# Kernel tuning notes

Measured on AMD Instinct MI355X. Metric: run time of the kernel, lower is better.

The kernel has to match this reference:

```python
import jax, jax.numpy as jnp
import numpy as np

B, S, C, V, LAT, NL = 256, 512, 256, 32, 256, 7
DILS = [1, 2, 4, 8, 16, 32, 64]
EPS = 1e-5


def setup_inputs() -> dict:
    key = jax.random.key(0)
    ks = jax.random.split(key, 24)
    s = 0.05
    inp = {
        "x": jax.random.randint(ks[0], (B, S), 0, V, dtype=jnp.int64 if jax.config.read("jax_enable_x64") else jnp.int32),
        "z": jax.random.normal(ks[1], (B, LAT), dtype=jnp.float32),
        "emb": jax.random.normal(ks[2], (V, C), dtype=jnp.float32) * s,
        "latent_W": jax.random.normal(ks[3], (LAT, C), dtype=jnp.float32) * s,
        "latent_b": jnp.zeros((C,), jnp.float32),
        "ln1_g": jnp.ones((NL, C), jnp.float32),
        "ln1_b": jnp.zeros((NL, C), jnp.float32),
        "w1": jax.random.normal(ks[4], (NL, C, C), jnp.float32) * s,
        "b1": jnp.zeros((NL, C), jnp.float32),
        "ln2_g": jnp.ones((NL, C), jnp.float32),
        "ln2_b": jnp.zeros((NL, C), jnp.float32),
        "wd": jax.random.normal(ks[5], (NL, 2, C, C), jnp.float32) * s,  # tap 0 = x[t-d], tap 1 = x[t]
        "bd": jnp.zeros((NL, C), jnp.float32),
        "ln3_g": jnp.ones((NL, C), jnp.float32),
        "ln3_b": jnp.zeros((NL, C), jnp.float32),
        "we": jax.random.normal(ks[6], (NL, C, C), jnp.float32) * s,
        "be": jnp.zeros((NL, C), jnp.float32),
        "wg": jax.random.normal(ks[7], (NL, C, C), jnp.float32) * s,
        "bg": jnp.zeros((NL, C), jnp.float32),
        "out_W": jax.random.normal(ks[8], (C, V), jnp.float32) * s,
        "out_b": jnp.zeros((V,), jnp.float32),
    }
    return inp


def _ln(h, g, b):
    mu = h.mean(-1, keepdims=True)
    var = jnp.mean((h - mu) ** 2, axis=-1, keepdims=True)
    return (h - mu) * jax.lax.rsqrt(var + EPS) * g + b


def _lrelu(h):
    return jnp.where(h >= 0, h, 0.01 * h)


def reference(x, z, emb, latent_W, latent_b, ln1_g, ln1_b, w1, b1,
              ln2_g, ln2_b, wd, bd, ln3_g, ln3_b, we, be, wg, bg,
              out_W, out_b):
    # channel-last layout [B, S, C] throughout (fuses away the torch transposes)
    h = emb[x] + (z @ latent_W + latent_b)[:, None, :]
    for i, d in enumerate(DILS):
        x_inp = h
        t = _lrelu(_ln(x_inp, ln1_g[i], ln1_b[i]))
        t = t @ w1[i] + b1[i]
        t = _lrelu(_ln(t, ln2_g[i], ln2_b[i]))
        # causal dilated conv, kernel=2: out[t] = W0*x[t-d] + W1*x[t]
        t_shift = jnp.pad(t, ((0, 0), (d, 0), (0, 0)))[:, :t.shape[1], :]
        t = t_shift @ wd[i, 0] + t @ wd[i, 1] + bd[i]
        t = _lrelu(_ln(t, ln3_g[i], ln3_b[i]))
        gated = (t @ we[i] + be[i]) * jax.nn.sigmoid(t @ wg[i] + bg[i])
        h = gated + x_inp
    logits = h @ out_W + out_b                      # [B, S, V]
    lp = jax.nn.log_softmax(logits, axis=-1)
    # gather log-prob of next token: lp[:, :-1, :] at x[:, 1:]
    return jnp.take_along_axis(lp[:, :-1, :], x[:, 1:, None], axis=2)[..., 0]
```

## Files before the change

### kernel.cpp

```cpp
#include <hip/hip_runtime.h>

typedef unsigned short u16;
typedef unsigned int   u32;
typedef __attribute__((ext_vector_type(8))) short short8;
typedef __attribute__((ext_vector_type(4))) float f32x4;

struct __align__(8) u16x4 { u16 x, y, z, w; };

#define NL 7
#define M_DIM 131072

__device__ __forceinline__ float b2f(u16 u) {
  union { float f; u32 i; } c; c.i = ((u32)u) << 16; return c.f;
}
__device__ __forceinline__ u16 f2b(float f) {
  union { float f; u32 i; } c; c.f = f;
  u32 r = c.i + 0x7FFFu + ((c.i >> 16) & 1u);
  return (u16)(r >> 16);
}
__device__ __forceinline__ void gload16(const void* g, void* l) {
  __builtin_amdgcn_global_load_lds((const __attribute__((address_space(1))) void*)g,
                                   (__attribute__((address_space(3))) void*)l, 16, 0, 0);
}


__global__ __launch_bounds__(256) void conv_w1_k(const float* __restrict__ w1, u16* __restrict__ wT) {
  int idx = blockIdx.x * 256 + threadIdx.x;
  int i = idx >> 16, rem = idx & 65535;
  int n = rem >> 8, k = rem & 255;
  wT[idx] = f2b(w1[(i << 16) + (k << 8) + n]);
}

__global__ __launch_bounds__(256) void conv_wd_k(const float* __restrict__ wd, u16* __restrict__ wT) {
  int idx = blockIdx.x * 256 + threadIdx.x;
  int i = idx / 131072, rem = idx & 131071;
  int n = rem >> 9, k2 = rem & 511;
  int tap = k2 >> 8, k = k2 & 255;
  wT[idx] = f2b(wd[(((i * 2 + tap) << 8) + k) * 256 + n]);
}

__global__ __launch_bounds__(256) void conv_weg_k(const float* __restrict__ we, const float* __restrict__ wg,
                                                  u16* __restrict__ wT) {
  int idx = blockIdx.x * 256 + threadIdx.x;
  int i = idx / 131072, rem = idx & 131071;
  int src = rem >> 16, n = (rem >> 8) & 255, k = rem & 255;
  const float* W = src ? wg : we;
  wT[idx] = f2b(W[((i << 8) + k) * 256 + n]);
}

__global__ __launch_bounds__(256) void conv_wo_k(const float* __restrict__ outW, u16* __restrict__ wTo) {
  int idx = blockIdx.x * 256 + threadIdx.x;
  int v = idx >> 8, k = idx & 255;
  wTo[idx] = f2b(outW[k * 32 + v]);
}


__global__ __launch_bounds__(256) void zlat_k(const float* __restrict__ z, const float* __restrict__ W,
                                              const float* __restrict__ bias, float* __restrict__ zlat) {
  int b = blockIdx.x, c = threadIdx.x;
  float acc = bias[c];
  for (int l = 0; l < 256; ++l) acc += z[b * 256 + l] * W[l * 256 + c];
  zlat[b * 256 + c] = acc;
}


__global__ __launch_bounds__(256) void embed_k(const int* __restrict__ x, const float* __restrict__ emb,
                                               const float* __restrict__ zlat, u16* __restrict__ h) {
  int wave = threadIdx.x >> 6, lane = threadIdx.x & 63;
  int r = blockIdx.x * 4 + wave;
  int c = lane * 4;
  int tok = x[r];
  int bi = r >> 9;
  float4 ev = *(const float4*)&emb[tok * 256 + c];
  float4 zv = *(const float4*)&zlat[bi * 256 + c];
  u16x4 hb;
  hb.x = f2b(ev.x + zv.x); hb.y = f2b(ev.y + zv.y);
  hb.z = f2b(ev.z + zv.z); hb.w = f2b(ev.w + zv.w);
  *(u16x4*)&h[(long)r * 256 + c] = hb;
}


__global__ __launch_bounds__(256, 2) void gemm1_k(
    const u16* __restrict__ h, const u16* __restrict__ WT,
    const float* __restrict__ ln1g, const float* __restrict__ ln1b,
    const float* __restrict__ bias,
    const float* __restrict__ ln2g, const float* __restrict__ ln2b,
    u16* __restrict__ V)
{
  __shared__ __align__(16) u16 lA[64 * 264];
  __shared__ __align__(16) u16 lB[256 * 32];
  __shared__ float pS[64][4], pQ[64][4];
  __shared__ float muA[64], rsA[64];
  const int tid = threadIdx.x;
  const int lane = tid & 63;
  const int wv = tid >> 6;
  const int wc = wv * 64;
  const int m0 = blockIdx.x * 64;
  const int rA = tid >> 2;
  const int cSw = ((((tid & 3) - ((tid >> 3) & 3)) & 3)) * 8;
  const int lr = lane & 15;
  const int quad = lane >> 4;
  const int lq = quad * 8;
  const int sw = ((quad + ((lr >> 1) & 3)) & 3) * 8;

  {
    const int half = lane >> 5, l5 = lane & 31;
    float4 ga = *(const float4*)&ln1g[l5 * 8];
    float4 gb = *(const float4*)&ln1g[l5 * 8 + 4];
    float4 ba = *(const float4*)&ln1b[l5 * 8];
    float4 bb = *(const float4*)&ln1b[l5 * 8 + 4];
    #pragma unroll 4
    for (int it = 0; it < 8; ++it) {
      int row = wv * 16 + it * 2 + half;
      uint4 hv = *(const uint4*)(h + (long)(m0 + row) * 256 + l5 * 8);
      float v0 = b2f((u16)(hv.x & 0xffff)), v1 = b2f((u16)(hv.x >> 16));
      float v2 = b2f((u16)(hv.y & 0xffff)), v3 = b2f((u16)(hv.y >> 16));
      float v4 = b2f((u16)(hv.z & 0xffff)), v5 = b2f((u16)(hv.z >> 16));
      float v6 = b2f((u16)(hv.w & 0xffff)), v7 = b2f((u16)(hv.w >> 16));
      float s = v0 + v1 + v2 + v3 + v4 + v5 + v6 + v7;
      float q = v0*v0 + v1*v1 + v2*v2 + v3*v3 + v4*v4 + v5*v5 + v6*v6 + v7*v7;
      #pragma unroll
      for (int o = 1; o < 32; o <<= 1) { s += __shfl_xor(s, o); q += __shfl_xor(q, o); }
      float mu = s * 0.00390625f;
      float var = q * 0.00390625f - mu * mu;
      float rs = rsqrtf(var + 1e-5f);
      float y0 = (v0 - mu) * rs * ga.x + ba.x; y0 = y0 >= 0.f ? y0 : 0.01f * y0;
      float y1 = (v1 - mu) * rs * ga.y + ba.y; y1 = y1 >= 0.f ? y1 : 0.01f * y1;
      float y2 = (v2 - mu) * rs * ga.z + ba.z; y2 = y2 >= 0.f ? y2 : 0.01f * y2;
      float y3 = (v3 - mu) * rs * ga.w + ba.w; y3 = y3 >= 0.f ? y3 : 0.01f * y3;
      float y4 = (v4 - mu) * rs * gb.x + bb.x; y4 = y4 >= 0.f ? y4 : 0.01f * y4;
      float y5 = (v5 - mu) * rs * gb.y + bb.y; y5 = y5 >= 0.f ? y5 : 0.01f * y5;
      float y6 = (v6 - mu) * rs * gb.z + bb.z; y6 = y6 >= 0.f ? y6 : 0.01f * y6;
      float y7 = (v7 - mu) * rs * gb.w + bb.w; y7 = y7 >= 0.f ? y7 : 0.01f * y7;
      uint4 ov;
      ov.x = (u32)f2b(y0) | ((u32)f2b(y1) << 16);
      ov.y = (u32)f2b(y2) | ((u32)f2b(y3) << 16);
      ov.z = (u32)f2b(y4) | ((u32)f2b(y5) << 16);
      ov.w = (u32)f2b(y6) | ((u32)f2b(y7) << 16);
      *(uint4*)&lA[row * 264 + l5 * 8] = ov;
    }
  }

  f32x4 acc[4][4];
  #pragma unroll
  for (int i = 0; i < 4; ++i)
    #pragma unroll
    for (int j = 0; j < 4; ++j) {
      acc[i][j][0] = 0.f; acc[i][j][1] = 0.f; acc[i][j][2] = 0.f; acc[i][j][3] = 0.f;
    }

  for (int kt = 0; kt < 8; ++kt) {
    const int kk = kt * 32;
    const long bofs = (long)rA * 256 + kk + cSw;
    #pragma unroll
    for (int j = 0; j < 4; ++j)
      gload16(WT + bofs + (long)(64 * j) * 256, &lB[tid * 8 + j * 2048]);
    __syncthreads();

    short8 af[4], bfr[4];
    #pragma unroll
    for (int mt = 0; mt < 4; ++mt)
      af[mt] = *(const short8*)&lA[(mt * 16 + lr) * 264 + kk + lq];
    #pragma unroll
    for (int nt = 0; nt < 4; ++nt)
      bfr[nt] = *(const short8*)&lB[(wc + nt * 16 + lr) * 32 + sw];
    #pragma unroll
    for (int mt = 0; mt < 4; ++mt)
      #pragma unroll
      for (int nt = 0; nt < 4; ++nt)
        acc[mt][nt] = __builtin_amdgcn_mfma_f32_16x16x32_bf16(af[mt], bfr[nt], acc[mt][nt], 0, 0, 0);
    __syncthreads();
  }

  float biasv[4], gv[4], bv[4];
  #pragma unroll
  for (int nt = 0; nt < 4; ++nt) {
    int n = wc + nt * 16 + lr;
    biasv[nt] = bias[n]; gv[nt] = ln2g[n]; bv[nt] = ln2b[n];
  }
  #pragma unroll
  for (int mt = 0; mt < 4; ++mt)
    #pragma unroll
    for (int r = 0; r < 4; ++r) {
      float s = 0.f, q = 0.f;
      #pragma unroll
      for (int nt = 0; nt < 4; ++nt) {
        float v = acc[mt][nt][r] + biasv[nt];
        acc[mt][nt][r] = v;
        s += v; q += v * v;
      }
      #pragma unroll
      for (int o = 1; o < 16; o <<= 1) { s += __shfl_xor(s, o); q += __shfl_xor(q, o); }
      if (lr == 0) { pS[mt * 16 + quad * 4 + r][wv] = s; pQ[mt * 16 + quad * 4 + r][wv] = q; }
    }
  __syncthreads();
  if (tid < 64) {
    float S = pS[tid][0] + pS[tid][1] + pS[tid][2] + pS[tid][3];
    float Q = pQ[tid][0] + pQ[tid][1] + pQ[tid][2] + pQ[tid][3];
    float mu = S * 0.00390625f;
    float var = Q * 0.00390625f - mu * mu;
    muA[tid] = mu; rsA[tid] = rsqrtf(var + 1e-5f);
  }
  __syncthreads();
  #pragma unroll
  for (int mt = 0; mt < 4; ++mt)
    #pragma unroll
    for (int r = 0; r < 4; ++r) {
      int row = mt * 16 + quad * 4 + r;
      float mu = muA[row], rs = rsA[row];
      #pragma unroll
      for (int nt = 0; nt < 4; ++nt) {
        float y = (acc[mt][nt][r] - mu) * rs * gv[nt] + bv[nt];
        y = y >= 0.f ? y : 0.01f * y;
        V[(long)(m0 + row) * 256 + wc + nt * 16 + lr] = f2b(y);
      }
    }
}


__global__ __launch_bounds__(512, 4) void gemm_ln_k(
    const u16* __restrict__ A, const u16* __restrict__ WT, int Ktot, int dil,
    const float* __restrict__ bias, const float* __restrict__ g, const float* __restrict__ b,
    u16* __restrict__ Out)
{
  __shared__ u16 lA[128 * 32];
  __shared__ u16 lB[256 * 32];
  __shared__ float pS[128][4], pQ[128][4];
  __shared__ float muA[128], rsA[128];
  const int tid = threadIdx.x;
  const int lane = tid & 63;
  const int wv = tid >> 6;
  const int mw = wv >> 2;
  const int nw = wv & 3;
  const int m0 = blockIdx.x * 128;
  const int rA = tid >> 2;
  const int cSw = ((((tid & 3) - ((tid >> 3) & 3)) & 3)) * 8;
  const int mm = m0 + rA;
  const int s1 = mm & 511;
  const bool fixBlk = (dil > 0) && ((m0 & 511) == 0);
  const int lr = lane & 15;
  const int quad = lane >> 4;
  const int sw = ((quad + ((lr >> 1) & 3)) & 3) * 8;

  f32x4 acc[4][4];
  #pragma unroll
  for (int i = 0; i < 4; ++i)
    #pragma unroll
    for (int j = 0; j < 4; ++j) {
      acc[i][j][0] = 0.f; acc[i][j][1] = 0.f; acc[i][j][2] = 0.f; acc[i][j][3] = 0.f;
    }

  const int nkt = Ktot >> 5;
  for (int kt = 0; kt < nkt; ++kt) {
    const int kk = (kt & 7) * 32;
    int r = mm;
    if (dil > 0 && kt < 8) r = (s1 >= dil) ? (mm - dil) : mm;
    gload16(A + (long)r * 256 + kk + cSw, &lA[tid * 8]);
    const u16* bSrc = WT + kt * 32 + cSw;
    gload16(bSrc + (long)rA * Ktot,         &lB[tid * 8]);
    gload16(bSrc + (long)(rA + 128) * Ktot, &lB[tid * 8 + 4096]);
    __syncthreads();

    if (fixBlk && kt < 8) {
      if (rA < dil) {
        uint4 zz; zz.x = 0; zz.y = 0; zz.z = 0; zz.w = 0;
        *(uint4*)&lA[rA * 32 + (tid & 3) * 8] = zz;
      }
      __syncthreads();
    }

    short8 af[4], bfr[4];
    #pragma unroll
    for (int mt = 0; mt < 4; ++mt)
      af[mt] = *(const short8*)&lA[(mw * 64 + mt * 16 + lr) * 32 + sw];
    #pragma unroll
    for (int nt = 0; nt < 4; ++nt)
      bfr[nt] = *(const short8*)&lB[(nw * 64 + nt * 16 + lr) * 32 + sw];
    #pragma unroll
    for (int mt = 0; mt < 4; ++mt)
      #pragma unroll
      for (int nt = 0; nt < 4; ++nt)
        acc[mt][nt] = __builtin_amdgcn_mfma_f32_16x16x32_bf16(af[mt], bfr[nt], acc[mt][nt], 0, 0, 0);
    __syncthreads();
  }

  float biasv[4], gv[4], bv[4];
  #pragma unroll
  for (int nt = 0; nt < 4; ++nt) {
    int n = nw * 64 + nt * 16 + lr;
    biasv[nt] = bias[n]; gv[nt] = g[n]; bv[nt] = b[n];
  }
  #pragma unroll
  for (int mt = 0; mt < 4; ++mt)
    #pragma unroll
    for (int r = 0; r < 4; ++r) {
      float s = 0.f, q = 0.f;
      #pragma unroll
      for (int nt = 0; nt < 4; ++nt) {
        float v = acc[mt][nt][r] + biasv[nt];
        acc[mt][nt][r] = v;
        s += v; q += v * v;
      }
      #pragma unroll
      for (int off = 1; off < 16; off <<= 1) {
        s += __shfl_xor(s, off); q += __shfl_xor(q, off);
      }
      if (lr == 0) {
        int row = mw * 64 + mt * 16 + quad * 4 + r;
        pS[row][nw] = s; pQ[row][nw] = q;
      }
    }
  __syncthreads();
  if (tid < 128) {
    float S = pS[tid][0] + pS[tid][1] + pS[tid][2] + pS[tid][3];
    float Q = pQ[tid][0] + pQ[tid][1] + pQ[tid][2] + pQ[tid][3];
    float mu = S * 0.00390625f;
    float var = Q * 0.00390625f - mu * mu;
    muA[tid] = mu; rsA[tid] = rsqrtf(var + 1e-5f);
  }
  __syncthreads();
  #pragma unroll
  for (int mt = 0; mt < 4; ++mt)
    #pragma unroll
    for (int r = 0; r < 4; ++r) {
      int row = mw * 64 + mt * 16 + quad * 4 + r;
      float mu = muA[row], rs = rsA[row];
      #pragma unroll
      for (int nt = 0; nt < 4; ++nt) {
        float y = (acc[mt][nt][r] - mu) * rs * gv[nt] + bv[nt];
        y = y >= 0.f ? y : 0.01f * y;
        Out[(long)(m0 + row) * 256 + nw * 64 + nt * 16 + lr] = f2b(y);
      }
    }
}


__global__ __launch_bounds__(256, 2) void gate_k(
    const u16* __restrict__ P, const u16* __restrict__ WTe, const u16* __restrict__ WTg,
    const float* __restrict__ be, const float* __restrict__ bg, u16* __restrict__ h)
{
  __shared__ u16 lA[64 * 32];
  __shared__ u16 lBe[256 * 32];
  __shared__ u16 lBg[256 * 32];
  const int tid = threadIdx.x;
  const int lane = tid & 63;
  const int wv = tid >> 6;
  const int wc = wv * 64;
  const int m0 = blockIdx.x * 64;
  const int rA = tid >> 2;
  const int cSw = ((((tid & 3) - ((tid >> 3) & 3)) & 3)) * 8;
  const int lr = lane & 15;
  const int quad = lane >> 4;
  const int sw = ((quad + ((lr >> 1) & 3)) & 3) * 8;

  f32x4 accE[4][4], accG[4][4];
  #pragma unroll
  for (int i = 0; i < 4; ++i)
    #pragma unroll
    for (int j = 0; j < 4; ++j) {
      accE[i][j][0] = 0.f; accE[i][j][1] = 0.f; accE[i][j][2] = 0.f; accE[i][j][3] = 0.f;
      accG[i][j][0] = 0.f; accG[i][j][1] = 0.f; accG[i][j][2] = 0.f; accG[i][j][3] = 0.f;
    }

  for (int kt = 0; kt < 8; ++kt) {
    const int kk = kt * 32;
    gload16(P + (long)(m0 + rA) * 256 + kk + cSw, &lA[tid * 8]);
    const long bofs = (long)rA * 256 + kk + cSw;
    #pragma unroll
    for (int j = 0; j < 4; ++j) {
      gload16(WTe + bofs + (long)(64 * j) * 256, &lBe[tid * 8 + j * 2048]);
      gload16(WTg + bofs + (long)(64 * j) * 256, &lBg[tid * 8 + j * 2048]);
    }
    __syncthreads();

    short8 af[4], bfe[4], bfg[4];
    #pragma unroll
    for (int mt = 0; mt < 4; ++mt)
      af[mt] = *(const short8*)&lA[(mt * 16 + lr) * 32 + sw];
    #pragma unroll
    for (int nt = 0; nt < 4; ++nt) {
      bfe[nt] = *(const short8*)&lBe[(wc + nt * 16 + lr) * 32 + sw];
      bfg[nt] = *(const short8*)&lBg[(wc + nt * 16 + lr) * 32 + sw];
    }
    #pragma unroll
    for (int mt = 0; mt < 4; ++mt)
      #pragma unroll
      for (int nt = 0; nt < 4; ++nt) {
        accE[mt][nt] = __builtin_amdgcn_mfma_f32_16x16x32_bf16(af[mt], bfe[nt], accE[mt][nt], 0, 0, 0);
        accG[mt][nt] = __builtin_amdgcn_mfma_f32_16x16x32_bf16(af[mt], bfg[nt], accG[mt][nt], 0, 0, 0);
      }
    __syncthreads();
  }

  float bev[4], bgv[4];
  #pragma unroll
  for (int nt = 0; nt < 4; ++nt) {
    int n = wc + nt * 16 + lr;
    bev[nt] = be[n]; bgv[nt] = bg[n];
  }
  #pragma unroll
  for (int mt = 0; mt < 4; ++mt)
    #pragma unroll
    for (int r = 0; r < 4; ++r) {
      int row = mt * 16 + quad * 4 + r;
      long off = (long)(m0 + row) * 256;
      #pragma unroll
      for (int nt = 0; nt < 4; ++nt) {
        int n = wc + nt * 16 + lr;
        float e = accE[mt][nt][r] + bev[nt];
        float gg = accG[mt][nt][r] + bgv[nt];
        float hn = e * (1.f / (1.f + expf(-gg))) + b2f(h[off + n]);
        h[off + n] = f2b(hn);
      }
    }
}


__global__ __launch_bounds__(256) void final_k(const u16* __restrict__ h, const u16* __restrict__ WTo,
                                               const float* __restrict__ outb, const int* __restrict__ x,
                                               float* __restrict__ out) {
  __shared__ u16 lW[32 * 264];
  const int tid = threadIdx.x;
  const int lane = tid & 63;
  const int wv = tid >> 6;
  const int mBase = blockIdx.x * 256 + wv * 64;

  #pragma unroll
  for (int j = 0; j < 4; ++j) {
    int chunk = tid + 256 * j;
    int v = chunk >> 5, k8 = chunk & 31;
    uint4 w4 = *(const uint4*)(WTo + v * 256 + k8 * 8);
    *(uint4*)&lW[v * 264 + k8 * 8] = w4;
  }
  __syncthreads();

  const int lq = (lane >> 4) * 8;
  const int lr = lane & 15;
  const int quad = lane >> 4;

  f32x4 acc[4][2];
  #pragma unroll
  for (int mt = 0; mt < 4; ++mt) {
    acc[mt][0][0] = 0.f; acc[mt][0][1] = 0.f; acc[mt][0][2] = 0.f; acc[mt][0][3] = 0.f;
    acc[mt][1][0] = 0.f; acc[mt][1][1] = 0.f; acc[mt][1][2] = 0.f; acc[mt][1][3] = 0.f;
  }

  for (int kt = 0; kt < 8; ++kt) {
    short8 bf0 = *(const short8*)&lW[lr * 264 + kt * 32 + lq];
    short8 bf1 = *(const short8*)&lW[(16 + lr) * 264 + kt * 32 + lq];
    #pragma unroll
    for (int mt = 0; mt < 4; ++mt) {
      short8 af = *(const short8*)(h + (long)(mBase + mt * 16 + lr) * 256 + kt * 32 + lq);
      acc[mt][0] = __builtin_amdgcn_mfma_f32_16x16x32_bf16(af, bf0, acc[mt][0], 0, 0, 0);
      acc[mt][1] = __builtin_amdgcn_mfma_f32_16x16x32_bf16(af, bf1, acc[mt][1], 0, 0, 0);
    }
  }

  float ob0 = outb[lr], ob1 = outb[16 + lr];
  #pragma unroll
  for (int mt = 0; mt < 4; ++mt)
    #pragma unroll
    for (int r = 0; r < 4; ++r) {
      int row = mBase + mt * 16 + quad * 4 + r;
      float lo = acc[mt][0][r] + ob0;
      float hi = acc[mt][1][r] + ob1;
      float mx = fmaxf(lo, hi);
      #pragma unroll
      for (int o = 1; o < 16; o <<= 1) mx = fmaxf(mx, __shfl_xor(mx, o));
      float se = expf(lo - mx) + expf(hi - mx);
      #pragma unroll
      for (int o = 1; o < 16; o <<= 1) se += __shfl_xor(se, o);
      int s = row & 511;
      int xa = (s == 511) ? row : (row + 1);
      int tok = x[xa];
      float lg = (tok < 16) ? lo : hi;
      float lp = lg - mx - logf(se);
      if (s != 511 && lr == (tok & 15))
        out[(row >> 9) * 511 + s] = lp;
    }
}


extern "C" void kernel_launch(void* const* d_in, const int* in_sizes, int n_in,
                              void* d_out, int out_size, void* d_ws, size_t ws_size,
                              hipStream_t stream) {
  const int*   x    = (const int*)d_in[0];
  const float* z    = (const float*)d_in[1];
  const float* emb  = (const float*)d_in[2];
  const float* latW = (const float*)d_in[3];
  const float* latb = (const float*)d_in[4];
  const float* ln1g = (const float*)d_in[5];
  const float* ln1b = (const float*)d_in[6];
  const float* w1   = (const float*)d_in[7];
  const float* b1   = (const float*)d_in[8];
  const float* ln2g = (const float*)d_in[9];
  const float* ln2b = (const float*)d_in[10];
  const float* wd   = (const float*)d_in[11];
  const float* bd   = (const float*)d_in[12];
  const float* ln3g = (const float*)d_in[13];
  const float* ln3b = (const float*)d_in[14];
  const float* we   = (const float*)d_in[15];
  const float* be   = (const float*)d_in[16];
  const float* wg   = (const float*)d_in[17];
  const float* bg   = (const float*)d_in[18];
  const float* outW = (const float*)d_in[19];
  const float* outb = (const float*)d_in[20];

  char* ws = (char*)d_ws;
  u16*   h    = (u16*)(ws + 0);
  u16*   bufA = (u16*)(ws + 67108864);
  u16*   bufB = (u16*)(ws + 134217728);
  float* zlat = (float*)(ws + 201326592);
  u16*   wT1  = (u16*)(ws + 201588736);
  u16*   wTd  = (u16*)(ws + 202506240);
  u16*   wTeg = (u16*)(ws + 204341248);
  u16*   wTo  = (u16*)(ws + 206176256);

  conv_w1_k <<<1792, 256, 0, stream>>>(w1, wT1);
  conv_wd_k <<<3584, 256, 0, stream>>>(wd, wTd);
  conv_weg_k<<<3584, 256, 0, stream>>>(we, wg, wTeg);
  conv_wo_k <<<32, 256, 0, stream>>>(outW, wTo);
  zlat_k    <<<256, 256, 0, stream>>>(z, latW, latb, zlat);
  embed_k   <<<M_DIM / 4, 256, 0, stream>>>(x, emb, zlat, h);

  for (int i = 0; i < NL; ++i) {
    int d = 1 << i;
    gemm1_k<<<M_DIM / 64, 256, 0, stream>>>(
        h, wT1 + i * 65536, ln1g + i * 256, ln1b + i * 256, b1 + i * 256,
        ln2g + i * 256, ln2b + i * 256, bufA);
    gemm_ln_k<<<M_DIM / 128, 512, 0, stream>>>(
        bufA, wTd + i * 131072, 512, d, bd + i * 256, ln3g + i * 256, ln3b + i * 256, bufB);
    gate_k<<<M_DIM / 64, 256, 0, stream>>>(
        bufB, wTeg + i * 131072, wTeg + i * 131072 + 65536, be + i * 256, bg + i * 256, h);
  }

  final_k<<<M_DIM / 256, 256, 0, stream>>>(h, wTo, outb, x, (float*)d_out);
}
```

Baseline: 1.475 ms.

## Fuse dilated-conv LN GEMM with gated GEMM, keep intermediate in LDS

Merges the dilated conv GEMM with its LN3 epilogue and the gate/residual GEMM into one kernel per layer. The normalized conv output stays in LDS for a 64-row tile and feeds the gate GEMM directly, so the bufB write and re-read through global memory goes away. Weight tiles are now loaded into a shared staging buffer that is prefetched one step ahead of the MFMAs, overlapping loads with compute. In exchange the tile shrinks from 128 to 64 rows with 256 threads. LDS use rises to about 66KB per block, which may limit occupancy, and conv weights are reread by twice as many blocks.

```diff
diff --git a/kernel.cpp b/kernel.cpp
--- a/kernel.cpp
+++ b/kernel.cpp
@@ -218,130 +218,20 @@
 }
 
 
-__global__ __launch_bounds__(512, 4) void gemm_ln_k(
-    const u16* __restrict__ A, const u16* __restrict__ WT, int Ktot, int dil,
-    const float* __restrict__ bias, const float* __restrict__ g, const float* __restrict__ b,
-    u16* __restrict__ Out)
+__global__ __launch_bounds__(256, 2) void conv_gate_k(
+    const u16* __restrict__ A,
+    const u16* __restrict__ WTd,
+    int dil,
+    const float* __restrict__ bd3, const float* __restrict__ g3, const float* __restrict__ bb3,
+    const u16* __restrict__ WTe, const u16* __restrict__ WTg,
+    const float* __restrict__ bev_, const float* __restrict__ bgv_,
+    u16* __restrict__ h)
 {
-  __shared__ u16 lA[128 * 32];
-  __shared__ u16 lB[256 * 32];
-  __shared__ float pS[128][4], pQ[128][4];
-  __shared__ float muA[128], rsA[128];
-  const int tid = threadIdx.x;
-  const int lane = tid & 63;
-  const int wv = tid >> 6;
-  const int mw = wv >> 2;
-  const int nw = wv & 3;
-  const int m0 = blockIdx.x * 128;
-  const int rA = tid >> 2;
-  const int cSw = ((((tid & 3) - ((tid >> 3) & 3)) & 3)) * 8;
-  const int mm = m0 + rA;
-  const int s1 = mm & 511;
-  const bool fixBlk = (dil > 0) && ((m0 & 511) == 0);
-  const int lr = lane & 15;
-  const int quad = lane >> 4;
-  const int sw = ((quad + ((lr >> 1) & 3)) & 3) * 8;
-
-  f32x4 acc[4][4];
-  #pragma unroll
-  for (int i = 0; i < 4; ++i)
-    #pragma unroll
-    for (int j = 0; j < 4; ++j) {
-      acc[i][j][0] = 0.f; acc[i][j][1] = 0.f; acc[i][j][2] = 0.f; acc[i][j][3] = 0.f;
-    }
-
-  const int nkt = Ktot >> 5;
-  for (int kt = 0; kt < nkt; ++kt) {
-    const int kk = (kt & 7) * 32;
-    int r = mm;
-    if (dil > 0 && kt < 8) r = (s1 >= dil) ? (mm - dil) : mm;
-    gload16(A + (long)r * 256 + kk + cSw, &lA[tid * 8]);
-    const u16* bSrc = WT + kt * 32 + cSw;
-    gload16(bSrc + (long)rA * Ktot,         &lB[tid * 8]);
-    gload16(bSrc + (long)(rA + 128) * Ktot, &lB[tid * 8 + 4096]);
-    __syncthreads();
-
-    if (fixBlk && kt < 8) {
-      if (rA < dil) {
-        uint4 zz; zz.x = 0; zz.y = 0; zz.z = 0; zz.w = 0;
-        *(uint4*)&lA[rA * 32 + (tid & 3) * 8] = zz;
-      }
-      __syncthreads();
-    }
-
-    short8 af[4], bfr[4];
-    #pragma unroll
-    for (int mt = 0; mt < 4; ++mt)
-      af[mt] = *(const short8*)&lA[(mw * 64 + mt * 16 + lr) * 32 + sw];
-    #pragma unroll
-    for (int nt = 0; nt < 4; ++nt)
-      bfr[nt] = *(const short8*)&lB[(nw * 64 + nt * 16 + lr) * 32 + sw];
-    #pragma unroll
-    for (int mt = 0; mt < 4; ++mt)
-      #pragma unroll
-      for (int nt = 0; nt < 4; ++nt)
-        acc[mt][nt] = __builtin_amdgcn_mfma_f32_16x16x32_bf16(af[mt], bfr[nt], acc[mt][nt], 0, 0, 0);
-    __syncthreads();
-  }
-
-  float biasv[4], gv[4], bv[4];
-  #pragma unroll
-  for (int nt = 0; nt < 4; ++nt) {
-    int n = nw * 64 + nt * 16 + lr;
-    biasv[nt] = bias[n]; gv[nt] = g[n]; bv[nt] = b[n];
-  }
-  #pragma unroll
-  for (int mt = 0; mt < 4; ++mt)
-    #pragma unroll
-    for (int r = 0; r < 4; ++r) {
-      float s = 0.f, q = 0.f;
-      #pragma unroll
-      for (int nt = 0; nt < 4; ++nt) {
-        float v = acc[mt][nt][r] + biasv[nt];
-        acc[mt][nt][r] = v;
-        s += v; q += v * v;
-      }
-      #pragma unroll
-      for (int off = 1; off < 16; off <<= 1) {
-        s += __shfl_xor(s, off); q += __shfl_xor(q, off);
-      }
-      if (lr == 0) {
-        int row = mw * 64 + mt * 16 + quad * 4 + r;
-        pS[row][nw] = s; pQ[row][nw] = q;
-      }
-    }
-  __syncthreads();
-  if (tid < 128) {
-    float S = pS[tid][0] + pS[tid][1] + pS[tid][2] + pS[tid][3];
-    float Q = pQ[tid][0] + pQ[tid][1] + pQ[tid][2] + pQ[tid][3];
-    float mu = S * 0.00390625f;
-    float var = Q * 0.00390625f - mu * mu;
-    muA[tid] = mu; rsA[tid] = rsqrtf(var + 1e-5f);
-  }
-  __syncthreads();
-  #pragma unroll
-  for (int mt = 0; mt < 4; ++mt)
-    #pragma unroll
-    for (int r = 0; r < 4; ++r) {
-      int row = mw * 64 + mt * 16 + quad * 4 + r;
-      float mu = muA[row], rs = rsA[row];
-      #pragma unroll
-      for (int nt = 0; nt < 4; ++nt) {
-        float y = (acc[mt][nt][r] - mu) * rs * gv[nt] + bv[nt];
-        y = y >= 0.f ? y : 0.01f * y;
-        Out[(long)(m0 + row) * 256 + nw * 64 + nt * 16 + lr] = f2b(y);
-      }
-    }
-}
-
-
-__global__ __launch_bounds__(256, 2) void gate_k(
-    const u16* __restrict__ P, const u16* __restrict__ WTe, const u16* __restrict__ WTg,
-    const float* __restrict__ be, const float* __restrict__ bg, u16* __restrict__ h)
-{
-  __shared__ u16 lA[64 * 32];
-  __shared__ u16 lBe[256 * 32];
-  __shared__ u16 lBg[256 * 32];
+  __shared__ __align__(16) u16 pT[64 * 264];
+  __shared__ __align__(16) u16 stg[16384];
+  __shared__ float pS[64][4], pQ[64][4];
+  __shared__ float muA[64], rsA[64];
+
   const int tid = threadIdx.x;
   const int lane = tid & 63;
   const int wv = tid >> 6;
@@ -351,7 +241,116 @@
   const int cSw = ((((tid & 3) - ((tid >> 3) & 3)) & 3)) * 8;
   const int lr = lane & 15;
   const int quad = lane >> 4;
+  const int lq = quad * 8;
   const int sw = ((quad + ((lr >> 1) & 3)) & 3) * 8;
+  const int mm = m0 + rA;
+  const int s1 = mm & 511;
+  const bool fixBlk = (m0 & 511) == 0;
+
+  f32x4 acc[4][4];
+  #pragma unroll
+  for (int i = 0; i < 4; ++i)
+    #pragma unroll
+    for (int j = 0; j < 4; ++j) {
+      acc[i][j][0] = 0.f; acc[i][j][1] = 0.f; acc[i][j][2] = 0.f; acc[i][j][3] = 0.f;
+    }
+
+#define STAGE_P1(KT) do {                                                        \
+    const int kt_ = (KT);                                                        \
+    const int kk_ = (kt_ & 7) * 32;                                              \
+    const int r_ = (kt_ < 8 && s1 >= dil) ? (mm - dil) : mm;                     \
+    gload16(A + (long)r_ * 256 + kk_ + cSw, &stg[tid * 8]);                      \
+    const u16* bSrc_ = WTd + kt_ * 32 + cSw;                                     \
+    gload16(bSrc_ + (long)rA * 512,         &stg[2048 + tid * 8]);               \
+    gload16(bSrc_ + (long)(rA + 64) * 512,  &stg[2048 + tid * 8 + 2048]);        \
+    gload16(bSrc_ + (long)(rA + 128) * 512, &stg[2048 + tid * 8 + 4096]);        \
+    gload16(bSrc_ + (long)(rA + 192) * 512, &stg[2048 + tid * 8 + 6144]);        \
+  } while (0)
+
+  STAGE_P1(0);
+  __syncthreads();
+
+  for (int kt = 0; kt < 16; ++kt) {
+    if (fixBlk && kt < 8) {
+      if (rA < dil) { uint4 zz; zz.x = 0; zz.y = 0; zz.z = 0; zz.w = 0; *(uint4*)&stg[tid * 8] = zz; }
+      __syncthreads();
+    }
+    short8 af[4], bfr[4];
+    #pragma unroll
+    for (int mt = 0; mt < 4; ++mt)
+      af[mt] = *(const short8*)&stg[(mt * 16 + lr) * 32 + sw];
+    #pragma unroll
+    for (int nt = 0; nt < 4; ++nt)
+      bfr[nt] = *(const short8*)&stg[2048 + (wc + nt * 16 + lr) * 32 + sw];
+    __syncthreads();
+    if (kt < 15) STAGE_P1(kt + 1);
+    #pragma unroll
+    for (int mt = 0; mt < 4; ++mt)
+      #pragma unroll
+      for (int nt = 0; nt < 4; ++nt)
+        acc[mt][nt] = __builtin_amdgcn_mfma_f32_16x16x32_bf16(af[mt], bfr[nt], acc[mt][nt], 0, 0, 0);
+    __syncthreads();
+  }
+#undef STAGE_P1
+
+#define STAGE_P2(KT) do {                                                        \
+    const long bofs_ = (long)rA * 256 + (KT) * 32 + cSw;                         \
+    gload16(WTe + bofs_,              &stg[tid * 8]);                            \
+    gload16(WTe + bofs_ + 64L * 256,  &stg[tid * 8 + 2048]);                     \
+    gload16(WTe + bofs_ + 128L * 256, &stg[tid * 8 + 4096]);                     \
+    gload16(WTe + bofs_ + 192L * 256, &stg[tid * 8 + 6144]);                     \
+    gload16(WTg + bofs_,              &stg[8192 + tid * 8]);                     \
+    gload16(WTg + bofs_ + 64L * 256,  &stg[8192 + tid * 8 + 2048]);              \
+    gload16(WTg + bofs_ + 128L * 256, &stg[8192 + tid * 8 + 4096]);              \
+    gload16(WTg + bofs_ + 192L * 256, &stg[8192 + tid * 8 + 6144]);              \
+  } while (0)
+
+  STAGE_P2(0);
+
+  float b3v[4], g3v[4], o3v[4];
+  #pragma unroll
+  for (int nt = 0; nt < 4; ++nt) {
+    int n = wc + nt * 16 + lr;
+    b3v[nt] = bd3[n]; g3v[nt] = g3[n]; o3v[nt] = bb3[n];
+  }
+  #pragma unroll
+  for (int mt = 0; mt < 4; ++mt)
+    #pragma unroll
+    for (int r = 0; r < 4; ++r) {
+      float s = 0.f, q = 0.f;
+      #pragma unroll
+      for (int nt = 0; nt < 4; ++nt) {
+        float v = acc[mt][nt][r] + b3v[nt];
+        acc[mt][nt][r] = v;
+        s += v; q += v * v;
+      }
+      #pragma unroll
+      for (int o = 1; o < 16; o <<= 1) { s += __shfl_xor(s, o); q += __shfl_xor(q, o); }
+      if (lr == 0) { pS[mt * 16 + quad * 4 + r][wv] = s; pQ[mt * 16 + quad * 4 + r][wv] = q; }
+    }
+  __syncthreads();
+  if (tid < 64) {
+    float S = pS[tid][0] + pS[tid][1] + pS[tid][2] + pS[tid][3];
+    float Q = pQ[tid][0] + pQ[tid][1] + pQ[tid][2] + pQ[tid][3];
+    float mu = S * 0.00390625f;
+    float var = Q * 0.00390625f - mu * mu;
+    muA[tid] = mu; rsA[tid] = rsqrtf(var + 1e-5f);
+  }
+  __syncthreads();
+  #pragma unroll
+  for (int mt = 0; mt < 4; ++mt)
+    #pragma unroll
+    for (int r = 0; r < 4; ++r) {
+      int row = mt * 16 + quad * 4 + r;
+      float mu = muA[row], rs = rsA[row];
+      #pragma unroll
+      for (int nt = 0; nt < 4; ++nt) {
+        float y = (acc[mt][nt][r] - mu) * rs * g3v[nt] + o3v[nt];
+        y = y >= 0.f ? y : 0.01f * y;
+        pT[row * 264 + wc + nt * 16 + lr] = f2b(y);
+      }
+    }
+  __syncthreads();
 
   f32x4 accE[4][4], accG[4][4];
   #pragma unroll
@@ -364,39 +363,33 @@
 
   for (int kt = 0; kt < 8; ++kt) {
     const int kk = kt * 32;
-    gload16(P + (long)(m0 + rA) * 256 + kk + cSw, &lA[tid * 8]);
-    const long bofs = (long)rA * 256 + kk + cSw;
-    #pragma unroll
-    for (int j = 0; j < 4; ++j) {
-      gload16(WTe + bofs + (long)(64 * j) * 256, &lBe[tid * 8 + j * 2048]);
-      gload16(WTg + bofs + (long)(64 * j) * 256, &lBg[tid * 8 + j * 2048]);
+    short8 paf[4], bfe[4], bfg[4];
+    #pragma unroll
+    for (int mt = 0; mt < 4; ++mt)
+      paf[mt] = *(const short8*)&pT[(mt * 16 + lr) * 264 + kk + lq];
+    #pragma unroll
+    for (int nt = 0; nt < 4; ++nt) {
+      bfe[nt] = *(const short8*)&stg[(wc + nt * 16 + lr) * 32 + sw];
+      bfg[nt] = *(const short8*)&stg[8192 + (wc + nt * 16 + lr) * 32 + sw];
     }
     __syncthreads();
-
-    short8 af[4], bfe[4], bfg[4];
+    if (kt < 7) STAGE_P2(kt + 1);
     #pragma unroll
     for (int mt = 0; mt < 4; ++mt)
-      af[mt] = *(const short8*)&lA[(mt * 16 + lr) * 32 + sw];
-    #pragma unroll
-    for (int nt = 0; nt < 4; ++nt) {
-      bfe[nt] = *(const short8*)&lBe[(wc + nt * 16 + lr) * 32 + sw];
-      bfg[nt] = *(const short8*)&lBg[(wc + nt * 16 + lr) * 32 + sw];
-    }
-    #pragma unroll
-    for (int mt = 0; mt < 4; ++mt)
       #pragma unroll
       for (int nt = 0; nt < 4; ++nt) {
-        accE[mt][nt] = __builtin_amdgcn_mfma_f32_16x16x32_bf16(af[mt], bfe[nt], accE[mt][nt], 0, 0, 0);
-        accG[mt][nt] = __builtin_amdgcn_mfma_f32_16x16x32_bf16(af[mt], bfg[nt], accG[mt][nt], 0, 0, 0);
+        accE[mt][nt] = __builtin_amdgcn_mfma_f32_16x16x32_bf16(paf[mt], bfe[nt], accE[mt][nt], 0, 0, 0);
+        accG[mt][nt] = __builtin_amdgcn_mfma_f32_16x16x32_bf16(paf[mt], bfg[nt], accG[mt][nt], 0, 0, 0);
       }
     __syncthreads();
   }
+#undef STAGE_P2
 
   float bev[4], bgv[4];
   #pragma unroll
   for (int nt = 0; nt < 4; ++nt) {
     int n = wc + nt * 16 + lr;
-    bev[nt] = be[n]; bgv[nt] = bg[n];
+    bev[nt] = bev_[n]; bgv[nt] = bgv_[n];
   }
   #pragma unroll
   for (int mt = 0; mt < 4; ++mt)
@@ -509,7 +502,6 @@
   char* ws = (char*)d_ws;
   u16*   h    = (u16*)(ws + 0);
   u16*   bufA = (u16*)(ws + 67108864);
-  u16*   bufB = (u16*)(ws + 134217728);
   float* zlat = (float*)(ws + 201326592);
   u16*   wT1  = (u16*)(ws + 201588736);
   u16*   wTd  = (u16*)(ws + 202506240);
@@ -528,10 +520,11 @@
     gemm1_k<<<M_DIM / 64, 256, 0, stream>>>(
         h, wT1 + i * 65536, ln1g + i * 256, ln1b + i * 256, b1 + i * 256,
         ln2g + i * 256, ln2b + i * 256, bufA);
-    gemm_ln_k<<<M_DIM / 128, 512, 0, stream>>>(
-        bufA, wTd + i * 131072, 512, d, bd + i * 256, ln3g + i * 256, ln3b + i * 256, bufB);
-    gate_k<<<M_DIM / 64, 256, 0, stream>>>(
-        bufB, wTeg + i * 131072, wTeg + i * 131072 + 65536, be + i * 256, bg + i * 256, h);
+    conv_gate_k<<<M_DIM / 64, 256, 0, stream>>>(
+        bufA, wTd + i * 131072, d,
+        bd + i * 256, ln3g + i * 256, ln3b + i * 256,
+        wTeg + i * 131072, wTeg + i * 131072 + 65536,
+        be + i * 256, bg + i * 256, h);
   }
 
   final_k<<<M_DIM / 256, 256, 0, stream>>>(h, wTo, outb, x, (float*)d_out);
```

Measured after the change: 1.467 ms. About the same (-0.5%).
